# Kernel tuning notes

Measured on AMD Instinct MI355X. Metric: run time of the kernel, lower is better.

The kernel has to match this reference:

```python
import jax, jax.numpy as jnp
import numpy as np

OUT, IN = 4096, 4096
GROUP = 128
N_GROUPS = IN // GROUP  # 32, remainder_cols == 0
BITS_PRIMARY = 4
BITS_RESIDUAL = 2
EPS = 1e-12


def setup_inputs() -> dict:
    key = jax.random.key(0)
    ks = jax.random.split(key, 6)
    return {
        "x": jax.random.normal(ks[0], (4, 2048, IN), dtype=jnp.float32),
        "norms_primary": jax.random.uniform(ks[1], (OUT, N_GROUPS), dtype=jnp.float32),
        "norms_residual": jax.random.uniform(ks[2], (OUT, N_GROUPS), dtype=jnp.float32),
        "bias": jax.random.normal(ks[3], (OUT,), dtype=jnp.float32),
        "idx_primary": jax.random.randint(ks[4], (OUT, N_GROUPS, GROUP), 0, 2 ** BITS_PRIMARY, dtype=jnp.int32),
        "idx_residual": jax.random.randint(ks[5], (OUT, N_GROUPS, GROUP), 0, 2 ** BITS_RESIDUAL, dtype=jnp.int32),
    }


def _dequant(idx, norms, bits):
    # Codebook: symmetric uniform levels in [-1, 1]; TurboQuant stores a
    # unit-direction per group (codes) plus its L2 norm (fp32 scale).
    levels = jnp.linspace(-1.0, 1.0, 2 ** bits, dtype=norms.dtype)
    q = levels[idx]                                             # [O, G, gs]
    unit = q * jax.lax.rsqrt(jnp.sum(q * q, axis=-1, keepdims=True) + EPS)
    w = norms[..., None] * unit                                 # [O, G, gs]
    return w.reshape(w.shape[0], -1)                            # [O, IN]


def reference(x, norms_primary, norms_residual, bias, idx_primary, idx_residual):
    # primary reconstruction + residual correction, then dense matmul
    w = _dequant(idx_primary, norms_primary, BITS_PRIMARY) \
        + _dequant(idx_residual, norms_residual, BITS_RESIDUAL)  # [OUT, IN]
    w = w.astype(x.dtype)
    # F.linear: y = x @ W^T + b
    return jnp.einsum('bsi,oi->bso', x, w) + bias.astype(x.dtype)
```

## Files before the change

kernel.cpp:

```cpp
#include <hip/hip_runtime.h>
#include <hip/hip_bf16.h>
#include <stdint.h>

#define OUT_DIM 4096
#define IN_DIM  4096
#define GROUPSZ 128
#define NGROUPS 32
#define M_TOTAL 8192
#define EPS_Q   1e-12f

#define BM 256
#define BN 256
#define BK 64
#define NT (IN_DIM / BK)

typedef float f32x4   __attribute__((ext_vector_type(4)));
typedef float float4v __attribute__((ext_vector_type(4)));
typedef short bf16x8  __attribute__((ext_vector_type(8)));

static __device__ __forceinline__ short f2bf(float f) {
    union { float f; unsigned u; } v; v.f = f;
    unsigned r = v.u + 0x7fffu + ((v.u >> 16) & 1u);
    return (short)(r >> 16);
}

#define GLOAD16(gp, lp) __builtin_amdgcn_global_load_lds( \
    (const __attribute__((address_space(1))) void*)(gp),  \
    (__attribute__((address_space(3))) void*)(lp), 16, 0, 0)

__global__ __launch_bounds__(256) void dequant_kernel(
    const float* __restrict__ norms_p, const float* __restrict__ norms_r,
    const int* __restrict__ idx_p, const int* __restrict__ idx_r,
    short* __restrict__ W)
{
    const int gid  = (int)((blockIdx.x * 256u + threadIdx.x) >> 6);
    const int lane = threadIdx.x & 63;
    const size_t base = (size_t)gid * GROUPSZ;

    const int ip0 = idx_p[base + lane];
    const int ip1 = idx_p[base + lane + 64];
    const int ir0 = idx_r[base + lane];
    const int ir1 = idx_r[base + lane + 64];

    const float qp0 = -1.f + (2.f / 15.f) * (float)ip0;
    const float qp1 = -1.f + (2.f / 15.f) * (float)ip1;
    const float qr0 = -1.f + (2.f / 3.f)  * (float)ir0;
    const float qr1 = -1.f + (2.f / 3.f)  * (float)ir1;

    float ssp = qp0 * qp0 + qp1 * qp1;
    float ssr = qr0 * qr0 + qr1 * qr1;
    #pragma unroll
    for (int m = 32; m >= 1; m >>= 1) {
        ssp += __shfl_xor(ssp, m);
        ssr += __shfl_xor(ssr, m);
    }
    const float sp = norms_p[gid] / sqrtf(ssp + EPS_Q);
    const float sr = norms_r[gid] / sqrtf(ssr + EPS_Q);

    W[base + lane]      = f2bf(qp0 * sp + qr0 * sr);
    W[base + lane + 64] = f2bf(qp1 * sp + qr1 * sr);
}

__global__ __launch_bounds__(256) void cast_kernel(
    const float* __restrict__ x, short* __restrict__ xb)
{
    const size_t i = ((size_t)blockIdx.x * 256u + threadIdx.x) * 8u;
    float4v a = *(const float4v*)(x + i);
    float4v b = *(const float4v*)(x + i + 4);
    bf16x8 o;
    o[0] = f2bf(a[0]); o[1] = f2bf(a[1]); o[2] = f2bf(a[2]); o[3] = f2bf(a[3]);
    o[4] = f2bf(b[0]); o[5] = f2bf(b[1]); o[6] = f2bf(b[2]); o[7] = f2bf(b[3]);
    *(bf16x8*)(xb + i) = o;
}

template<int HA, int HB>
__device__ __forceinline__ void mfma_quad(f32x4 (&acc)[2][2][4][2],
                                          const bf16x8 (&af)[4][2],
                                          const bf16x8 (&bf)[2][2]) {
#pragma unroll
    for (int m = 0; m < 4; ++m)
#pragma unroll
        for (int n = 0; n < 2; ++n)
#pragma unroll
            for (int kh = 0; kh < 2; ++kh)
                acc[HA][HB][m][n] = __builtin_amdgcn_mfma_f32_16x16x32_bf16(
                    af[m][kh], bf[n][kh], acc[HA][HB][m][n], 0, 0, 0);
}

static __device__ __forceinline__ void rd8(const short* base, int ck0, int ck1,
                                           bf16x8 (&f)[4][2]) {
#pragma unroll
    for (int m = 0; m < 4; ++m) {
        f[m][0] = *(const bf16x8*)(base + m * 1024 + ck0);
        f[m][1] = *(const bf16x8*)(base + m * 1024 + ck1);
    }
}

static __device__ __forceinline__ void rd4(const short* base, int ck0, int ck1,
                                           bf16x8 (&f)[2][2]) {
#pragma unroll
    for (int n = 0; n < 2; ++n) {
        f[n][0] = *(const bf16x8*)(base + n * 1024 + ck0);
        f[n][1] = *(const bf16x8*)(base + n * 1024 + ck1);
    }
}

#define BARRIER()  asm volatile("s_barrier" ::: "memory")
#define SCHEDBAR() __builtin_amdgcn_sched_barrier(0)
#define LGKMC(N)   do { asm volatile("s_waitcnt lgkmcnt(" #N ")" ::: "memory"); \
                        SCHEDBAR(); } while (0)
#define WAITV(N)   asm volatile("s_waitcnt vmcnt(" #N ")" ::: "memory")

__global__ __launch_bounds__(512, 2) void gemm_kernel(
    const short* __restrict__ Ag,
    const short* __restrict__ Bg,
    const float* __restrict__ bias,
    float* __restrict__ C)
{
    __shared__ short lds[65536];

    const int tid  = threadIdx.x;
    const int lane = tid & 63;
    const int wid  = tid >> 6;
    const int wr   = wid >> 2;
    const int wc   = wid & 3;
    const int fr   = lane & 15;
    const int lq   = lane >> 4;

    const int nwg = gridDim.x;
    const int cpx = nwg >> 3;
    const int wg  = ((int)blockIdx.x & 7) * cpx + ((int)blockIdx.x >> 3);
    const int ntile = wg & 15;
    const int mtile = wg >> 4;
    const uint32_t brow = (uint32_t)mtile * BM;
    const uint32_t bcol = (uint32_t)ntile * BN;

    const uint32_t sr_ = (uint32_t)(tid >> 3);
    const uint32_t gc_ = (uint32_t)((tid & 7) ^ ((tid >> 3) & 7));
    const uint32_t aOffB = (brow + sr_) * IN_DIM + gc_ * 8;
    const uint32_t bOffB = (bcol + sr_) * IN_DIM + gc_ * 8;

    auto stage = [&](const short* M, uint32_t baseOff, uint32_t extra, short* dstRegion) {
        GLOAD16(M + baseOff + extra,            dstRegion + tid * 8);
        GLOAD16(M + baseOff + extra + 262144u,  dstRegion + tid * 8 + 4096);
    };

    const int c0  = (lq ^ (fr & 7));
    const int ck0 = c0 * 8;
    const int ck1 = (c0 ^ 4) * 8;
    const int aRd = (wr * 64 + fr) * 64;
    const int bRd = (wc * 32 + fr) * 64;

    f32x4  acc[2][2][4][2] = {};
    bf16x8 af[4][2], af2[4][2], bf0[2][2], bf1[2][2];

    stage(Ag, aOffB, 0u,            lds);
    stage(Bg, bOffB, 0u,            lds + 16384);
    stage(Ag, aOffB, 524288u,       lds + 8192);
    stage(Bg, bOffB, 524288u,       lds + 24576);
    stage(Ag, aOffB, 64u,           lds + 32768);
    stage(Bg, bOffB, 64u,           lds + 32768 + 16384);
    WAITV(8);
    BARRIER();

#define TILE_BODY(T, PEND, STG0, STG1, STG2, STG3, WAIT_MID, WAIT_END, BAR_END, DO_TAIL) do { \
    short* sb = lds + (((T) & 1) ? 32768 : 0);                                \
    short* ob = lds + (((T) & 1) ? 0 : 32768);                                \
                \
    rd8(sb + aRd, ck0, ck1, af);                                              \
    rd4(sb + 16384 + bRd, ck0, ck1, bf0);                                     \
    if (STG0) stage(Ag, aOffB, 524288u + (uint32_t)((T) + 1) * 64u, ob + 8192); \
    SCHEDBAR();                                                               \
    if (PEND) {    \
        __builtin_amdgcn_s_setprio(1); mfma_quad<1,1>(acc, af2, bf1);         \
        __builtin_amdgcn_s_setprio(0);                                        \
    }                                                                         \
    LGKMC(0);                                                                 \
    __builtin_amdgcn_s_setprio(1); mfma_quad<0,0>(acc, af, bf0);              \
    __builtin_amdgcn_s_setprio(0);                                            \
    WAIT_MID;                                                                 \
    BARRIER();                                                                \
                             \
    rd4(sb + 24576 + bRd, ck0, ck1, bf1);                                     \
    SCHEDBAR();                                                               \
    rd8(sb + 8192 + aRd, ck0, ck1, af2);                                      \
    if (STG1) stage(Bg, bOffB, 524288u + (uint32_t)((T) + 1) * 64u, ob + 24576); \
    LGKMC(8);                     \
    __builtin_amdgcn_s_setprio(1); mfma_quad<0,1>(acc, af, bf1);              \
    __builtin_amdgcn_s_setprio(0);                                            \
    if (STG2) stage(Ag, aOffB, (uint32_t)((T) + 2) * 64u, sb);                \
    LGKMC(0);                    \
    __builtin_amdgcn_s_setprio(1); mfma_quad<1,0>(acc, af2, bf0);             \
    __builtin_amdgcn_s_setprio(0);                                            \
    if (STG3) stage(Bg, bOffB, (uint32_t)((T) + 2) * 64u, sb + 16384);        \
    if (DO_TAIL) {                   \
        __builtin_amdgcn_s_setprio(1); mfma_quad<1,1>(acc, af2, bf1);         \
        __builtin_amdgcn_s_setprio(0);                                        \
    }                                                                         \
    WAIT_END;                                                                 \
    if (BAR_END) BARRIER();                                                   \
} while (0)

    TILE_BODY(0, 0, 1, 1, 1, 1, WAITV(6), WAITV(8), 1, 0);
    #pragma unroll 1
    for (int t = 1; t < NT - 2; ++t) {
        TILE_BODY(t, 1, 1, 1, 1, 1, WAITV(6), WAITV(8), 1, 0);
    }
    TILE_BODY(NT - 2, 1, 1, 1, 0, 0, WAITV(6), WAITV(4), 1, 0);
    TILE_BODY(NT - 1, 1, 0, 0, 0, 0, WAITV(0), (void)0, 0, 1);
#undef TILE_BODY

    #pragma unroll
    for (int hA = 0; hA < 2; ++hA)
    #pragma unroll
    for (int hB = 0; hB < 2; ++hB)
    #pragma unroll
    for (int n = 0; n < 2; ++n) {
        const int col = (int)bcol + hB * 128 + wc * 32 + n * 16 + fr;
        const float bv = bias[col];
        #pragma unroll
        for (int m = 0; m < 4; ++m) {
            const size_t row0 = (size_t)brow + hA * 128 + wr * 64 + m * 16 + lq * 4;
            #pragma unroll
            for (int r = 0; r < 4; ++r)
                C[(row0 + r) * OUT_DIM + col] = acc[hA][hB][m][n][r] + bv;
        }
    }
}

extern "C" void kernel_launch(void* const* d_in, const int* in_sizes, int n_in,
                              void* d_out, int out_size, void* d_ws, size_t ws_size,
                              hipStream_t stream)
{
    const float* x        = (const float*)d_in[0];
    const float* norms_p  = (const float*)d_in[1];
    const float* norms_r  = (const float*)d_in[2];
    const float* bias     = (const float*)d_in[3];
    const int*   idx_p    = (const int*)d_in[4];
    const int*   idx_r    = (const int*)d_in[5];
    float*       out      = (float*)d_out;

    short* xb = (short*)d_ws;
    short* wq = (short*)d_ws + (size_t)M_TOTAL * IN_DIM;

    dequant_kernel<<<(OUT_DIM * NGROUPS) / 4, 256, 0, stream>>>(
        norms_p, norms_r, idx_p, idx_r, wq);

    cast_kernel<<<(int)(((size_t)M_TOTAL * IN_DIM) / (256 * 8)), 256, 0, stream>>>(x, xb);

    gemm_kernel<<<(M_TOTAL / BM) * (OUT_DIM / BN), 512, 0, stream>>>(xb, wq, bias, out);
}
```

Baseline: 279.0 us.

## Fuse fp32-to-bf16 activation cast into GEMM A-tile loading

Drops the separate cast kernel and its bf16 workspace. The GEMM now loads fp32 activations into registers, packs them to bf16 and writes them to LDS itself, while B tiles still use direct global-to-LDS loads. This removes one kernel launch and the write and reread of the 64MB bf16 copy of x. In exchange the GEMM reads twice the bytes for A from fp32, which is repeated across the 16 N-tiles, and gains extra VGPR pressure and a reworked wait and pipeline schedule.

Result: slower. 590.0 us (+111.5%).

```diff
diff --git a/kernel.cpp b/kernel.cpp
--- a/kernel.cpp
+++ b/kernel.cpp
@@ -17,6 +17,7 @@
 typedef float f32x4   __attribute__((ext_vector_type(4)));
 typedef float float4v __attribute__((ext_vector_type(4)));
 typedef short bf16x8  __attribute__((ext_vector_type(8)));
+typedef unsigned int u32x4 __attribute__((ext_vector_type(4)));
 
 static __device__ __forceinline__ short f2bf(float f) {
     union { float f; unsigned u; } v; v.f = f;
@@ -61,18 +62,6 @@
     W[base + lane + 64] = f2bf(qp1 * sp + qr1 * sr);
 }
 
-__global__ __launch_bounds__(256) void cast_kernel(
-    const float* __restrict__ x, short* __restrict__ xb)
-{
-    const size_t i = ((size_t)blockIdx.x * 256u + threadIdx.x) * 8u;
-    float4v a = *(const float4v*)(x + i);
-    float4v b = *(const float4v*)(x + i + 4);
-    bf16x8 o;
-    o[0] = f2bf(a[0]); o[1] = f2bf(a[1]); o[2] = f2bf(a[2]); o[3] = f2bf(a[3]);
-    o[4] = f2bf(b[0]); o[5] = f2bf(b[1]); o[6] = f2bf(b[2]); o[7] = f2bf(b[3]);
-    *(bf16x8*)(xb + i) = o;
-}
-
 template<int HA, int HB>
 __device__ __forceinline__ void mfma_quad(f32x4 (&acc)[2][2][4][2],
                                           const bf16x8 (&af)[4][2],
@@ -103,6 +92,15 @@
         f[n][0] = *(const bf16x8*)(base + n * 1024 + ck0);
         f[n][1] = *(const bf16x8*)(base + n * 1024 + ck1);
     }
+}
+
+static __device__ __forceinline__ u32x4 pk8(const f32x4& a, const f32x4& b) {
+    union { __hip_bfloat162 h[4]; u32x4 u; } p;
+    p.h[0] = __float22bfloat162_rn(float2{a[0], a[1]});
+    p.h[1] = __float22bfloat162_rn(float2{a[2], a[3]});
+    p.h[2] = __float22bfloat162_rn(float2{b[0], b[1]});
+    p.h[3] = __float22bfloat162_rn(float2{b[2], b[3]});
+    return p.u;
 }
 
 #define BARRIER()  asm volatile("s_barrier" ::: "memory")
@@ -112,7 +110,7 @@
 #define WAITV(N)   asm volatile("s_waitcnt vmcnt(" #N ")" ::: "memory")
 
 __global__ __launch_bounds__(512, 2) void gemm_kernel(
-    const short* __restrict__ Ag,
+    const float* __restrict__ Xf,
     const short* __restrict__ Bg,
     const float* __restrict__ bias,
     float* __restrict__ C)
@@ -137,12 +135,19 @@
 
     const uint32_t sr_ = (uint32_t)(tid >> 3);
     const uint32_t gc_ = (uint32_t)((tid & 7) ^ ((tid >> 3) & 7));
-    const uint32_t aOffB = (brow + sr_) * IN_DIM + gc_ * 8;
+    const float* aSrc = Xf + (size_t)(brow + sr_) * IN_DIM + gc_ * 8;
     const uint32_t bOffB = (bcol + sr_) * IN_DIM + gc_ * 8;
 
-    auto stage = [&](const short* M, uint32_t baseOff, uint32_t extra, short* dstRegion) {
-        GLOAD16(M + baseOff + extra,            dstRegion + tid * 8);
-        GLOAD16(M + baseOff + extra + 262144u,  dstRegion + tid * 8 + 4096);
+    auto stageB = [&](uint32_t extra, short* dstRegion) {
+        GLOAD16(Bg + bOffB + extra,            dstRegion + tid * 8);
+        GLOAD16(Bg + bOffB + extra + 262144u,  dstRegion + tid * 8 + 4096);
+    };
+    auto issueA = [&](uint32_t extra, f32x4 (&h)[4]) {
+        const float* p = aSrc + extra;
+        h[0] = *(const f32x4*)(p);
+        h[1] = *(const f32x4*)(p + 4);
+        h[2] = *(const f32x4*)(p + 262144u);
+        h[3] = *(const f32x4*)(p + 262144u + 4);
     };
 
     const int c0  = (lq ^ (fr & 7));
@@ -153,25 +158,42 @@
 
     f32x4  acc[2][2][4][2] = {};
     bf16x8 af[4][2], af2[4][2], bf0[2][2], bf1[2][2];
-
-    stage(Ag, aOffB, 0u,            lds);
-    stage(Bg, bOffB, 0u,            lds + 16384);
-    stage(Ag, aOffB, 524288u,       lds + 8192);
-    stage(Bg, bOffB, 524288u,       lds + 24576);
-    stage(Ag, aOffB, 64u,           lds + 32768);
-    stage(Bg, bOffB, 64u,           lds + 32768 + 16384);
+    f32x4  hA0n[4], hA1n[4];
+    u32x4  hA1pk0, hA1pk1;
+
+    issueA(0u,       hA0n);
+    issueA(524288u,  hA1n);
+    SCHEDBAR();
+    stageB(0u,       lds + 16384);
+    stageB(524288u,  lds + 24576);
+    SCHEDBAR();
     WAITV(8);
+    *(u32x4*)(lds + tid * 8)        = pk8(hA0n[0], hA0n[1]);
+    *(u32x4*)(lds + tid * 8 + 4096) = pk8(hA0n[2], hA0n[3]);
+    WAITV(2);
+    hA1pk0 = pk8(hA1n[0], hA1n[1]);
+    hA1pk1 = pk8(hA1n[2], hA1n[3]);
+    LGKMC(0);
     BARRIER();
 
-#define TILE_BODY(T, PEND, STG0, STG1, STG2, STG3, WAIT_MID, WAIT_END, BAR_END, DO_TAIL) do { \
+#define TILE_BODY(T, PEND, ISS, WAIT_MID, DO_TAIL, BAR_END) do {              \
     short* sb = lds + (((T) & 1) ? 32768 : 0);                                \
     short* ob = lds + (((T) & 1) ? 0 : 32768);                                \
-                \
+                    \
     rd8(sb + aRd, ck0, ck1, af);                                              \
     rd4(sb + 16384 + bRd, ck0, ck1, bf0);                                     \
-    if (STG0) stage(Ag, aOffB, 524288u + (uint32_t)((T) + 1) * 64u, ob + 8192); \
+    *(u32x4*)(sb + 8192 + tid * 8)        = hA1pk0;                           \
+    *(u32x4*)(sb + 8192 + tid * 8 + 4096) = hA1pk1;                           \
     SCHEDBAR();                                                               \
-    if (PEND) {    \
+    if (ISS) {                                                                \
+        issueA((uint32_t)((T) + 1) * 64u, hA0n);                              \
+        issueA(524288u + (uint32_t)((T) + 1) * 64u, hA1n);                    \
+        SCHEDBAR();                                                           \
+        stageB((uint32_t)((T) + 1) * 64u, ob + 16384);                        \
+        stageB(524288u + (uint32_t)((T) + 1) * 64u, ob + 24576);              \
+        SCHEDBAR();                                                           \
+    }                                                                         \
+    if (PEND) {                                                               \
         __builtin_amdgcn_s_setprio(1); mfma_quad<1,1>(acc, af2, bf1);         \
         __builtin_amdgcn_s_setprio(0);                                        \
     }                                                                         \
@@ -180,34 +202,38 @@
     __builtin_amdgcn_s_setprio(0);                                            \
     WAIT_MID;                                                                 \
     BARRIER();                                                                \
-                             \
+                                                                 \
     rd4(sb + 24576 + bRd, ck0, ck1, bf1);                                     \
     SCHEDBAR();                                                               \
     rd8(sb + 8192 + aRd, ck0, ck1, af2);                                      \
-    if (STG1) stage(Bg, bOffB, 524288u + (uint32_t)((T) + 1) * 64u, ob + 24576); \
     LGKMC(8);                     \
     __builtin_amdgcn_s_setprio(1); mfma_quad<0,1>(acc, af, bf1);              \
     __builtin_amdgcn_s_setprio(0);                                            \
-    if (STG2) stage(Ag, aOffB, (uint32_t)((T) + 2) * 64u, sb);                \
-    LGKMC(0);                    \
+    LGKMC(0);                                                                 \
     __builtin_amdgcn_s_setprio(1); mfma_quad<1,0>(acc, af2, bf0);             \
     __builtin_amdgcn_s_setprio(0);                                            \
-    if (STG3) stage(Bg, bOffB, (uint32_t)((T) + 2) * 64u, sb + 16384);        \
-    if (DO_TAIL) {                   \
+    if (ISS) {                                                                \
+        WAITV(8);                                         \
+        *(u32x4*)(ob + tid * 8)        = pk8(hA0n[0], hA0n[1]);               \
+        *(u32x4*)(ob + tid * 8 + 4096) = pk8(hA0n[2], hA0n[3]);               \
+        WAITV(2);              \
+        hA1pk0 = pk8(hA1n[0], hA1n[1]);                                       \
+        hA1pk1 = pk8(hA1n[2], hA1n[3]);                                       \
+    }                                                                         \
+    if (DO_TAIL) {                                                            \
         __builtin_amdgcn_s_setprio(1); mfma_quad<1,1>(acc, af2, bf1);         \
         __builtin_amdgcn_s_setprio(0);                                        \
     }                                                                         \
-    WAIT_END;                                                                 \
+    LGKMC(0);                                                                 \
     if (BAR_END) BARRIER();                                                   \
 } while (0)
 
-    TILE_BODY(0, 0, 1, 1, 1, 1, WAITV(6), WAITV(8), 1, 0);
+    TILE_BODY(0, 0, 1, WAITV(12), 0, 1);
     #pragma unroll 1
-    for (int t = 1; t < NT - 2; ++t) {
-        TILE_BODY(t, 1, 1, 1, 1, 1, WAITV(6), WAITV(8), 1, 0);
-    }
-    TILE_BODY(NT - 2, 1, 1, 1, 0, 0, WAITV(6), WAITV(4), 1, 0);
-    TILE_BODY(NT - 1, 1, 0, 0, 0, 0, WAITV(0), (void)0, 0, 1);
+    for (int t = 1; t <= NT - 2; ++t) {
+        TILE_BODY(t, 1, 1, WAITV(12), 0, 1);
+    }
+    TILE_BODY(NT - 1, 1, 0, WAITV(0), 1, 0);
 #undef TILE_BODY
 
     #pragma unroll
@@ -240,13 +266,10 @@
     const int*   idx_r    = (const int*)d_in[5];
     float*       out      = (float*)d_out;
 
-    short* xb = (short*)d_ws;
-    short* wq = (short*)d_ws + (size_t)M_TOTAL * IN_DIM;
+    short* wq = (short*)d_ws;
 
     dequant_kernel<<<(OUT_DIM * NGROUPS) / 4, 256, 0, stream>>>(
         norms_p, norms_r, idx_p, idx_r, wq);
 
-    cast_kernel<<<(int)(((size_t)M_TOTAL * IN_DIM) / (256 * 8)), 256, 0, stream>>>(x, xb);
-
-    gemm_kernel<<<(M_TOTAL / BM) * (OUT_DIM / BN), 512, 0, stream>>>(xb, wq, bias, out);
-}
+    gemm_kernel<<<(M_TOTAL / BM) * (OUT_DIM / BN), 512, 0, stream>>>(x, wq, bias, out);
+}
```
